# Performance work log

Measured on AMD Instinct MI355X. Metric: run time of the kernel, lower is better.

## Reference

```python
import jax, jax.numpy as jnp
import numpy as np

B, T, H, S = 2, 2048, 16, 64
EMB = H * S  # 1024


def layer_norm(x, g, b, eps=1e-5):
    mu = jnp.mean(x, axis=-1, keepdims=True)
    var = jnp.var(x, axis=-1, keepdims=True)
    return (x - mu) * jax.lax.rsqrt(var + eps) * g + b


def setup_inputs() -> dict:
    key = jax.random.key(0)
    ks = jax.random.split(key, 12)
    sc = 0.02
    return {
        "x": jax.random.normal(ks[0], (B, T, EMB), dtype=jnp.float32),
        "Wkqv": jax.random.normal(ks[1], (S, 3 * S), dtype=jnp.float32) * sc,
        "Wproj": jax.random.normal(ks[2], (EMB, EMB), dtype=jnp.float32) * sc,
        "g1": jnp.ones((EMB,), jnp.float32),
        "b1": jnp.zeros((EMB,), jnp.float32),
        "W1": jax.random.normal(ks[3], (EMB, 4 * EMB), dtype=jnp.float32) * sc,
        "bff1": jnp.zeros((4 * EMB,), jnp.float32),
        "W2": jax.random.normal(ks[4], (4 * EMB, EMB), dtype=jnp.float32) * sc,
        "bff2": jnp.zeros((EMB,), jnp.float32),
        "g2": jnp.ones((EMB,), jnp.float32),
        "b2": jnp.zeros((EMB,), jnp.float32),
    }


def reference(x, Wkqv, Wproj, g1, b1, W1, bff1, W2, bff2, g2, b2):
    Bb, Tt, _ = x.shape
    xh = x.reshape(Bb, Tt, H, S)                     # [B,T,H,S]
    kqv = jnp.einsum('bths,sd->bthd', xh, Wkqv)      # [B,T,H,3S], shared per-head weight
    k, q, v = jnp.split(kqv, 3, axis=-1)             # note order: k, q, v
    scores = jnp.einsum('bihk,bjhk->bijh', q, k) / jnp.sqrt(jnp.float32(S))
    att = jax.nn.softmax(scores, axis=2)             # softmax over key dim j
    res = jnp.einsum('btih,bihs->bths', att, v).reshape(Bb, Tt, EMB)
    mha = res @ Wproj                                # Linear(emb, emb, bias=False)
    x = layer_norm(x + mha, g1, b1)
    h = jax.nn.gelu(x @ W1 + bff1, approximate=False)
    ff = h @ W2 + bff2
    return layer_norm(x + ff, g2, b2)
```

## Files before the change

kernel.cpp:

```cpp
#include <hip/hip_runtime.h>
#include <hip/hip_bf16.h>
#include <math.h>

#define B_ 2
#define T_ 2048
#define H_ 16
#define S_ 64
#define EMB 1024
#define FF 4096
#define BT (B_*T_)
#define ROWS (B_*T_*H_)

typedef __attribute__((ext_vector_type(8))) short s16x8;
typedef __attribute__((ext_vector_type(4))) float f32x4;

struct P4 { unsigned short* p[4]; };

__device__ __forceinline__ unsigned short f2b(float f) {
    return __builtin_bit_cast(unsigned short, __float2bfloat16(f));
}
__device__ __forceinline__ float b2f(short u) {
    return __builtin_bit_cast(float, ((unsigned int)(unsigned short)u) << 16);
}

__device__ __forceinline__ void gl_lds16(const void* g, void* l) {
    __builtin_amdgcn_global_load_lds(
        (const __attribute__((address_space(1))) void*)g,
        (__attribute__((address_space(3))) void*)l, 16, 0, 0);
}

__device__ __forceinline__ f32x4 mfma16(s16x8 a, s16x8 b, f32x4 c) {
    return __builtin_amdgcn_mfma_f32_16x16x32_bf16(a, b, c, 0, 0, 0);
}

#define WAIT_VM8 0x0F78
#define WAIT_VM0 0x0F70

__global__ __launch_bounds__(256) void kqv_kernel(const float* __restrict__ x,
        const unsigned short* __restrict__ Wqt, unsigned short* __restrict__ K,
        unsigned short* __restrict__ Q, unsigned short* __restrict__ V) {
    const int tid = threadIdx.x;
    const int w = tid >> 6, lane = tid & 63;
    const int l15 = lane & 15, quad = lane >> 4;
    const long r0 = (long)blockIdx.x * 128 + w * 32;

    s16x8 af[2][2];
    #pragma unroll
    for (int mt = 0; mt < 2; ++mt)
        #pragma unroll
        for (int ks = 0; ks < 2; ++ks) {
            const float* xp = x + (r0 + mt*16 + l15) * 64 + ks*32 + quad*8;
            const float4 v0 = *(const float4*)xp;
            const float4 v1 = *(const float4*)(xp + 4);
            s16x8 a;
            a[0] = (short)f2b(v0.x); a[1] = (short)f2b(v0.y);
            a[2] = (short)f2b(v0.z); a[3] = (short)f2b(v0.w);
            a[4] = (short)f2b(v1.x); a[5] = (short)f2b(v1.y);
            a[6] = (short)f2b(v1.z); a[7] = (short)f2b(v1.w);
            af[mt][ks] = a;
        }

    #pragma unroll
    for (int nt = 0; nt < 12; ++nt) {
        const s16x8 b0 = *(const s16x8*)&Wqt[(nt*16 + l15)*64 + quad*8];
        const s16x8 b1 = *(const s16x8*)&Wqt[(nt*16 + l15)*64 + 32 + quad*8];
        f32x4 acc[2] = {};
        #pragma unroll
        for (int mt = 0; mt < 2; ++mt) {
            acc[mt] = mfma16(af[mt][0], b0, acc[mt]);
            acc[mt] = mfma16(af[mt][1], b1, acc[mt]);
        }
        unsigned short* dst = (nt < 4) ? K : (nt < 8) ? Q : V;
        const int c0 = (nt & 3) * 16 + l15;
        #pragma unroll
        for (int mt = 0; mt < 2; ++mt)
            #pragma unroll
            for (int r = 0; r < 4; ++r)
                dst[(r0 + mt*16 + quad*4 + r) * 64 + c0] = f2b(acc[mt][r]);
    }
}

__global__ __launch_bounds__(256) void vt_kernel(const unsigned short* __restrict__ V,
        unsigned short* __restrict__ VT) {
    __shared__ unsigned short Ts[64][72];
    const int tid = threadIdx.x;
    const int tt = blockIdx.x, bh = blockIdx.y;
    const int b = bh >> 4, h = bh & 15;
    const long vbase = ((long)b * (T_*H_) + h) * 64;
    #pragma unroll
    for (int i = 0; i < 2; ++i) {
        const int id = i * 256 + tid;
        const int tr = id >> 3, dc = (id & 7) * 8;
        const s16x8 v = *(const s16x8*)&V[vbase + (long)(tt*64 + tr)*1024 + dc];
        *(s16x8*)&Ts[tr][dc] = v;
    }
    __syncthreads();
    #pragma unroll
    for (int i = 0; i < 2; ++i) {
        const int id = i * 256 + tid;
        const int d = id >> 3, tc = (id & 7) * 8;
        s16x8 o;
        #pragma unroll
        for (int j = 0; j < 8; ++j) o[j] = (short)Ts[tc + j][d];
        *(s16x8*)&VT[((long)bh*64 + d)*2048 + tt*64 + tc] = o;
    }
}

__global__ __launch_bounds__(64, 2) void attn_kernel(const unsigned short* __restrict__ Q,
        const unsigned short* __restrict__ K, const unsigned short* __restrict__ VT,
        unsigned short* __restrict__ res) {
    __shared__ __align__(16) unsigned short Kbuf[2][2][32*32];
    __shared__ __align__(16) unsigned short Vbuf[2][64*32];
    __shared__ __align__(16) unsigned short Ps[32*36];
    const int lane = threadIdx.x;
    const int l15 = lane & 15, quad = lane >> 4;
    const int bid = blockIdx.x;
    const int qt = bid & 63, bh = bid >> 6;
    const int b = bh >> 4, h = bh & 15;
    const long base = ((long)b * (T_*H_) + h) * 64;
    const unsigned short* Qp = Q + base;
    const unsigned short* Kp = K + base;
    const unsigned short* Vp = VT + (long)bh * 64 * 2048;
    const int q0 = qt * 32;

    s16x8 qf[2][2];
    #pragma unroll
    for (int qq = 0; qq < 2; ++qq)
        #pragma unroll
        for (int ks = 0; ks < 2; ++ks) {
            const s16x8 raw = *(const s16x8*)&Qp[(long)(q0 + qq*16 + l15)*1024 + ks*32 + quad*8];
            s16x8 q;
            #pragma unroll
            for (int j = 0; j < 8; ++j) q[j] = (short)f2b(b2f(raw[j]) * 0.125f);
            qf[qq][ks] = q;
        }

    s16x8 onef;
    #pragma unroll
    for (int j = 0; j < 8; ++j) onef[j] = (short)0x3F80;

    f32x4 oacc[2][4] = {};
    f32x4 lacc[2] = {};

    const int j16 = lane >> 2;
    const int c8  = (lane & 3) * 8;

    auto stage = [&](int bufi, int kt) {
        const unsigned short* kg = Kp + (long)(kt*32) * 1024;
        char* kl = (char*)&Kbuf[bufi][0][0];
        gl_lds16(kg + (long)j16*1024 + c8,           kl +    0 + lane*16);
        gl_lds16(kg + (long)(j16+16)*1024 + c8,      kl + 1024 + lane*16);
        gl_lds16(kg + (long)j16*1024 + 32 + c8,      kl + 2048 + lane*16);
        gl_lds16(kg + (long)(j16+16)*1024 + 32 + c8, kl + 3072 + lane*16);
        const unsigned short* vg = Vp + kt*32 + c8;
        char* vl = (char*)&Vbuf[bufi][0];
        gl_lds16(vg + (long)(j16     )*2048, vl +    0 + lane*16);
        gl_lds16(vg + (long)(j16 + 16)*2048, vl + 1024 + lane*16);
        gl_lds16(vg + (long)(j16 + 32)*2048, vl + 2048 + lane*16);
        gl_lds16(vg + (long)(j16 + 48)*2048, vl + 3072 + lane*16);
    };

    auto compute = [&](int bufi) {
        f32x4 sT[2][2] = {};
        #pragma unroll
        for (int ks = 0; ks < 2; ++ks)
            #pragma unroll
            for (int jt = 0; jt < 2; ++jt) {
                const s16x8 kf = *(const s16x8*)&Kbuf[bufi][ks][(jt*16 + l15)*32 + quad*8];
                sT[jt][0] = mfma16(kf, qf[0][ks], sT[jt][0]);
                sT[jt][1] = mfma16(kf, qf[1][ks], sT[jt][1]);
            }
        #pragma unroll
        for (int jt = 0; jt < 2; ++jt)
            #pragma unroll
            for (int qq = 0; qq < 2; ++qq) {
                uint2 pk;
                pk.x = (unsigned int)f2b(__expf(sT[jt][qq][0]))
                     | ((unsigned int)f2b(__expf(sT[jt][qq][1])) << 16);
                pk.y = (unsigned int)f2b(__expf(sT[jt][qq][2]))
                     | ((unsigned int)f2b(__expf(sT[jt][qq][3])) << 16);
                *(uint2*)&Ps[(qq*16 + l15)*36 + jt*16 + quad*4] = pk;
            }
        s16x8 pf[2];
        #pragma unroll
        for (int qq = 0; qq < 2; ++qq) {
            pf[qq] = *(const s16x8*)&Ps[(qq*16 + l15)*36 + quad*8];
            lacc[qq] = mfma16(pf[qq], onef, lacc[qq]);
        }
        #pragma unroll
        for (int nt = 0; nt < 4; ++nt) {
            const s16x8 vf = *(const s16x8*)&Vbuf[bufi][(nt*16 + l15)*32 + quad*8];
            oacc[0][nt] = mfma16(pf[0], vf, oacc[0][nt]);
            oacc[1][nt] = mfma16(pf[1], vf, oacc[1][nt]);
        }
    };

    stage(0, 0);
    for (int kt = 0; kt < 63; ++kt) {
        stage((kt + 1) & 1, kt + 1);
        __builtin_amdgcn_s_waitcnt(WAIT_VM8);
        __builtin_amdgcn_sched_barrier(0);
        compute(kt & 1);
    }
    __builtin_amdgcn_s_waitcnt(WAIT_VM0);
    __builtin_amdgcn_sched_barrier(0);
    compute(1);

    #pragma unroll
    for (int qq = 0; qq < 2; ++qq)
        #pragma unroll
        for (int r = 0; r < 4; ++r) {
            const float inv = 1.f / lacc[qq][r];
            const int t = q0 + qq*16 + quad*4 + r;
            #pragma unroll
            for (int nt = 0; nt < 4; ++nt)
                res[((long)(b*T_ + t))*EMB + h*64 + nt*16 + l15] =
                    f2b(oacc[qq][nt][r] * inv);
        }
}

__global__ __launch_bounds__(256) void gemm_gelu(const unsigned short* __restrict__ A,
        const unsigned short* __restrict__ Bt, const float* __restrict__ bias,
        unsigned short* __restrict__ C, int M, int N, int Kd) {
    __shared__ __align__(16) unsigned short As[128 * 32];
    __shared__ __align__(16) unsigned short Bs[128 * 32];
    const int tid = threadIdx.x;
    const int w = tid >> 6, lane = tid & 63;
    const int l15 = lane & 15, quad = lane >> 4;
    const int wm = w >> 1, wn = w & 1;
    const int bn = blockIdx.x, bm = blockIdx.y;
    const int sr = lane >> 2, skq = lane & 3;
    f32x4 acc[4][4] = {};
    const long arow = (long)(bm*128 + w*32 + sr);
    const long brow = (long)(bn*128 + w*32 + sr);

    for (int kt = 0; kt < Kd; kt += 32) {
        gl_lds16(A  + (arow     )*Kd + kt + skq*8, (char*)As + (w*32     )*64 + lane*16);
        gl_lds16(A  + (arow + 16)*Kd + kt + skq*8, (char*)As + (w*32 + 16)*64 + lane*16);
        gl_lds16(Bt + (brow     )*Kd + kt + skq*8, (char*)Bs + (w*32     )*64 + lane*16);
        gl_lds16(Bt + (brow + 16)*Kd + kt + skq*8, (char*)Bs + (w*32 + 16)*64 + lane*16);
        __syncthreads();
        s16x8 af[4], bf[4];
        #pragma unroll
        for (int mt = 0; mt < 4; ++mt)
            af[mt] = *(const s16x8*)&As[(wm*64 + mt*16 + l15)*32 + quad*8];
        #pragma unroll
        for (int nt = 0; nt < 4; ++nt)
            bf[nt] = *(const s16x8*)&Bs[(wn*64 + nt*16 + l15)*32 + quad*8];
        #pragma unroll
        for (int mt = 0; mt < 4; ++mt)
            #pragma unroll
            for (int nt = 0; nt < 4; ++nt)
                acc[mt][nt] = mfma16(af[mt], bf[nt], acc[mt][nt]);
        __syncthreads();
    }

    #pragma unroll
    for (int mt = 0; mt < 4; ++mt) {
        const int row0 = bm*128 + wm*64 + mt*16 + quad*4;
        #pragma unroll
        for (int nt = 0; nt < 4; ++nt) {
            const int col = bn*128 + wn*64 + nt*16 + l15;
            const float bv = bias[col];
            #pragma unroll
            for (int r = 0; r < 4; ++r) {
                float v = acc[mt][nt][r] + bv;
                v = 0.5f * v * (1.f + erff(v * 0.70710678118654752440f));
                C[(long)(row0 + r)*N + col] = f2b(v);
            }
        }
    }
}

__global__ __launch_bounds__(256) void gemm_splitk(const unsigned short* __restrict__ A,
        const unsigned short* __restrict__ Bt, P4 parts, int M, int N, int Kd, int Ks) {
    __shared__ __align__(16) unsigned short As[128 * 32];
    __shared__ __align__(16) unsigned short Bs[128 * 32];
    const int tid = threadIdx.x;
    const int w = tid >> 6, lane = tid & 63;
    const int l15 = lane & 15, quad = lane >> 4;
    const int wm = w >> 1, wn = w & 1;
    const int bn = blockIdx.x, bm = blockIdx.y, s = blockIdx.z;
    const int sr = lane >> 2, skq = lane & 3;
    f32x4 acc[4][4] = {};
    const long arow = (long)(bm*128 + w*32 + sr);
    const long brow = (long)(bn*128 + w*32 + sr);
    const int k0 = s * Ks;

    for (int kt = k0; kt < k0 + Ks; kt += 32) {
        gl_lds16(A  + (arow     )*Kd + kt + skq*8, (char*)As + (w*32     )*64 + lane*16);
        gl_lds16(A  + (arow + 16)*Kd + kt + skq*8, (char*)As + (w*32 + 16)*64 + lane*16);
        gl_lds16(Bt + (brow     )*Kd + kt + skq*8, (char*)Bs + (w*32     )*64 + lane*16);
        gl_lds16(Bt + (brow + 16)*Kd + kt + skq*8, (char*)Bs + (w*32 + 16)*64 + lane*16);
        __syncthreads();
        s16x8 af[4], bf[4];
        #pragma unroll
        for (int mt = 0; mt < 4; ++mt)
            af[mt] = *(const s16x8*)&As[(wm*64 + mt*16 + l15)*32 + quad*8];
        #pragma unroll
        for (int nt = 0; nt < 4; ++nt)
            bf[nt] = *(const s16x8*)&Bs[(wn*64 + nt*16 + l15)*32 + quad*8];
        #pragma unroll
        for (int mt = 0; mt < 4; ++mt)
            #pragma unroll
            for (int nt = 0; nt < 4; ++nt)
                acc[mt][nt] = mfma16(af[mt], bf[nt], acc[mt][nt]);
        __syncthreads();
    }

    unsigned short* Cp = parts.p[s];
    #pragma unroll
    for (int mt = 0; mt < 4; ++mt) {
        const int row0 = bm*128 + wm*64 + mt*16 + quad*4;
        #pragma unroll
        for (int nt = 0; nt < 4; ++nt) {
            const int col = bn*128 + wn*64 + nt*16 + l15;
            #pragma unroll
            for (int r = 0; r < 4; ++r)
                Cp[(long)(row0 + r)*N + col] = f2b(acc[mt][nt][r]);
        }
    }
}

template <int P, int XBF>
__global__ __launch_bounds__(256) void ln_kernel(const void* __restrict__ xa,
        P4 parts, const float* __restrict__ addb, const float* __restrict__ g,
        const float* __restrict__ bia, float* __restrict__ out,
        unsigned short* __restrict__ outb) {
    const int row = blockIdx.x;
    const int tid = threadIdx.x;
    float4 v;
    if (XBF) {
        const ushort4 u = ((const ushort4*)xa)[(long)row * (EMB/4) + tid];
        v.x = b2f((short)u.x); v.y = b2f((short)u.y);
        v.z = b2f((short)u.z); v.w = b2f((short)u.w);
    } else {
        v = ((const float4*)xa)[(long)row * (EMB/4) + tid];
    }
    #pragma unroll
    for (int p = 0; p < P; ++p) {
        const ushort4 u = ((const ushort4*)(parts.p[p] + (long)row * EMB))[tid];
        v.x += b2f((short)u.x); v.y += b2f((short)u.y);
        v.z += b2f((short)u.z); v.w += b2f((short)u.w);
    }
    if (addb) {
        const float4 ab = ((const float4*)addb)[tid];
        v.x += ab.x; v.y += ab.y; v.z += ab.z; v.w += ab.w;
    }
    float s = v.x + v.y + v.z + v.w;
    float ss = v.x * v.x + v.y * v.y + v.z * v.z + v.w * v.w;
    #pragma unroll
    for (int off = 32; off > 0; off >>= 1) {
        s += __shfl_down(s, off, 64);
        ss += __shfl_down(ss, off, 64);
    }
    __shared__ float ls[4], lss[4];
    __shared__ float mean_s, rstd_s;
    const int wid = tid >> 6, lane = tid & 63;
    if (lane == 0) { ls[wid] = s; lss[wid] = ss; }
    __syncthreads();
    if (tid == 0) {
        const float S0 = ls[0] + ls[1] + ls[2] + ls[3];
        const float S2 = lss[0] + lss[1] + lss[2] + lss[3];
        const float mean = S0 * (1.f / EMB);
        const float var = S2 * (1.f / EMB) - mean * mean;
        mean_s = mean;
        rstd_s = rsqrtf(var + 1e-5f);
    }
    __syncthreads();
    const float mean = mean_s, rstd = rstd_s;
    const float4 gg = ((const float4*)g)[tid];
    const float4 bb = ((const float4*)bia)[tid];
    float4 o;
    o.x = (v.x - mean) * rstd * gg.x + bb.x;
    o.y = (v.y - mean) * rstd * gg.y + bb.y;
    o.z = (v.z - mean) * rstd * gg.z + bb.z;
    o.w = (v.w - mean) * rstd * gg.w + bb.w;
    if (out) ((float4*)(out + (long)row * EMB))[tid] = o;
    if (outb) {
        unsigned short* ob = outb + (long)row * EMB + tid * 4;
        ob[0] = f2b(o.x); ob[1] = f2b(o.y); ob[2] = f2b(o.z); ob[3] = f2b(o.w);
    }
}

__global__ __launch_bounds__(256) void transp_all(const float* __restrict__ Wp,
        const float* __restrict__ W1, const float* __restrict__ W2,
        const float* __restrict__ Wq, unsigned short* __restrict__ Wpt,
        unsigned short* __restrict__ W1t, unsigned short* __restrict__ W2t,
        unsigned short* __restrict__ Wqt) {
    int id = blockIdx.x;
    const float* W; unsigned short* Wt; int Kd, N, ntx;
    if (id < 1024)      {            W = Wp; Wt = Wpt; Kd = 1024; N = 1024; ntx = 32; }
    else if (id < 5120) { id -= 1024; W = W1; Wt = W1t; Kd = 1024; N = 4096; ntx = 128; }
    else if (id < 9216) { id -= 5120; W = W2; Wt = W2t; Kd = 4096; N = 1024; ntx = 32; }
    else                { id -= 9216; W = Wq; Wt = Wqt; Kd = 64;   N = 192;  ntx = 6;  }
    __shared__ float Ts[32][33];
    const int tid = threadIdx.x;
    const int n0 = (id % ntx) * 32, k0 = (id / ntx) * 32;
    const int r = tid >> 3, c4 = (tid & 7) * 4;
    const float4 v = *(const float4*)&W[(long)(k0 + r) * N + n0 + c4];
    Ts[r][c4] = v.x; Ts[r][c4 + 1] = v.y; Ts[r][c4 + 2] = v.z; Ts[r][c4 + 3] = v.w;
    __syncthreads();
    #pragma unroll
    for (int i = 0; i < 4; ++i)
        Wt[(long)(n0 + r) * Kd + k0 + c4 + i] = f2b(Ts[c4 + i][r]);
}

extern "C" void kernel_launch(void* const* d_in, const int* in_sizes, int n_in,
                              void* d_out, int out_size, void* d_ws, size_t ws_size,
                              hipStream_t stream) {
    (void)in_sizes; (void)n_in; (void)out_size;
    const float* x     = (const float*)d_in[0];
    const float* Wkqv  = (const float*)d_in[1];
    const float* Wproj = (const float*)d_in[2];
    const float* g1    = (const float*)d_in[3];
    const float* b1    = (const float*)d_in[4];
    const float* W1    = (const float*)d_in[5];
    const float* bff1  = (const float*)d_in[6];
    const float* W2    = (const float*)d_in[7];
    const float* bff2  = (const float*)d_in[8];
    const float* g2    = (const float*)d_in[9];
    const float* b2    = (const float*)d_in[10];
    float* out = (float*)d_out;
    char* ws = (char*)d_ws;

    const size_t MB = 1u << 20;
    unsigned short* Qb   = (unsigned short*)(ws + 0 * MB);
    unsigned short* Kb   = (unsigned short*)(ws + 8 * MB);
    unsigned short* Vb   = (unsigned short*)(ws + 16 * MB);
    unsigned short* resb = (unsigned short*)(ws + 24 * MB);
    unsigned short* hb   = (unsigned short*)(ws + 8 * MB);
    unsigned short* VTb  = (unsigned short*)(ws + 40 * MB);
    unsigned short* mp0  = (unsigned short*)(ws + 40 * MB);
    unsigned short* mp1  = (unsigned short*)(ws + 48 * MB);
    unsigned short* x1b  = Qb;
    unsigned short* Wpt  = (unsigned short*)(ws + 72 * MB);
    unsigned short* W1t  = (unsigned short*)(ws + 74 * MB);
    unsigned short* W2t  = (unsigned short*)(ws + 82 * MB);
    unsigned short* Wqt  = (unsigned short*)(ws + 90 * MB);
    unsigned short* fp2  = (unsigned short*)(ws + 91 * MB);
    unsigned short* fp3  = (unsigned short*)(ws + 99 * MB);
    const bool big = ws_size >= 108 * MB;

    transp_all<<<dim3(9228), 256, 0, stream>>>(Wproj, W1, W2, Wkqv, Wpt, W1t, W2t, Wqt);

    kqv_kernel<<<dim3(ROWS/128), 256, 0, stream>>>(x, Wqt, Kb, Qb, Vb);
    vt_kernel<<<dim3(T_/64, B_*H_), 256, 0, stream>>>(Vb, VTb);
    attn_kernel<<<dim3(2048), 64, 0, stream>>>(Qb, Kb, VTb, resb);
    P4 mp; mp.p[0] = mp0; mp.p[1] = mp1; mp.p[2] = nullptr; mp.p[3] = nullptr;
    gemm_splitk<<<dim3(EMB/128, BT/128, 2), 256, 0, stream>>>(resb, Wpt, mp, BT, EMB, EMB, EMB/2);
    ln_kernel<2, 0><<<dim3(BT), 256, 0, stream>>>(x, mp, nullptr, g1, b1, nullptr, x1b);
    gemm_gelu<<<dim3(FF/128, BT/128), 256, 0, stream>>>(x1b, W1t, bff1, hb, BT, FF, EMB);
    if (big) {
        P4 fp; fp.p[0] = mp0; fp.p[1] = mp1; fp.p[2] = fp2; fp.p[3] = fp3;
        gemm_splitk<<<dim3(EMB/128, BT/128, 4), 256, 0, stream>>>(hb, W2t, fp, BT, EMB, FF, FF/4);
        ln_kernel<4, 1><<<dim3(BT), 256, 0, stream>>>(x1b, fp, bff2, g2, b2, out, nullptr);
    } else {
        P4 fp; fp.p[0] = mp0; fp.p[1] = mp1; fp.p[2] = nullptr; fp.p[3] = nullptr;
        gemm_splitk<<<dim3(EMB/128, BT/128, 2), 256, 0, stream>>>(hb, W2t, fp, BT, EMB, FF, FF/2);
        ln_kernel<2, 1><<<dim3(BT), 256, 0, stream>>>(x1b, fp, bff2, g2, b2, out, nullptr);
    }
}
```

Before: 361.3 us.

## Load attention K/V tiles directly into registers with double-buffered prefetch

Replaces the LDS staging of K and V tiles (global_load_lds plus explicit waitcnt and sched barriers) with direct global-to-register loads. Two register sets are ping-ponged so the next tile's loads are issued while the current tile is computed. The occupancy hint in launch_bounds is dropped, and the bf16 pack switches from rounding to truncation of the exp values. This cuts LDS traffic and the manual wait bookkeeping, but uses more VGPRs, leaves latency hiding to the compiler, and truncation slightly changes numerics.

```diff
diff --git a/kernel.cpp b/kernel.cpp
--- a/kernel.cpp
+++ b/kernel.cpp
@@ -22,6 +22,11 @@
 __device__ __forceinline__ float b2f(short u) {
     return __builtin_bit_cast(float, ((unsigned int)(unsigned short)u) << 16);
 }
+__device__ __forceinline__ unsigned int pk2t(float a, float b) {
+    const unsigned ua = __builtin_bit_cast(unsigned, a);
+    const unsigned ub = __builtin_bit_cast(unsigned, b);
+    return (ub & 0xffff0000u) | (ua >> 16);
+}
 
 __device__ __forceinline__ void gl_lds16(const void* g, void* l) {
     __builtin_amdgcn_global_load_lds(
@@ -32,9 +37,6 @@
 __device__ __forceinline__ f32x4 mfma16(s16x8 a, s16x8 b, f32x4 c) {
     return __builtin_amdgcn_mfma_f32_16x16x32_bf16(a, b, c, 0, 0, 0);
 }
-
-#define WAIT_VM8 0x0F78
-#define WAIT_VM0 0x0F70
 
 __global__ __launch_bounds__(256) void kqv_kernel(const float* __restrict__ x,
         const unsigned short* __restrict__ Wqt, unsigned short* __restrict__ K,
@@ -106,12 +108,10 @@
     }
 }
 
-__global__ __launch_bounds__(64, 2) void attn_kernel(const unsigned short* __restrict__ Q,
+__global__ __launch_bounds__(64) void attn_kernel(const unsigned short* __restrict__ Q,
         const unsigned short* __restrict__ K, const unsigned short* __restrict__ VT,
         unsigned short* __restrict__ res) {
-    __shared__ __align__(16) unsigned short Kbuf[2][2][32*32];
-    __shared__ __align__(16) unsigned short Vbuf[2][64*32];
-    __shared__ __align__(16) unsigned short Ps[32*36];
+    __shared__ __align__(16) unsigned short Ps[32 * 36];
     const int lane = threadIdx.x;
     const int l15 = lane & 15, quad = lane >> 4;
     const int bid = blockIdx.x;
@@ -142,43 +142,41 @@
     f32x4 oacc[2][4] = {};
     f32x4 lacc[2] = {};
 
-    const int j16 = lane >> 2;
-    const int c8  = (lane & 3) * 8;
-
-    auto stage = [&](int bufi, int kt) {
-        const unsigned short* kg = Kp + (long)(kt*32) * 1024;
-        char* kl = (char*)&Kbuf[bufi][0][0];
-        gl_lds16(kg + (long)j16*1024 + c8,           kl +    0 + lane*16);
-        gl_lds16(kg + (long)(j16+16)*1024 + c8,      kl + 1024 + lane*16);
-        gl_lds16(kg + (long)j16*1024 + 32 + c8,      kl + 2048 + lane*16);
-        gl_lds16(kg + (long)(j16+16)*1024 + 32 + c8, kl + 3072 + lane*16);
-        const unsigned short* vg = Vp + kt*32 + c8;
-        char* vl = (char*)&Vbuf[bufi][0];
-        gl_lds16(vg + (long)(j16     )*2048, vl +    0 + lane*16);
-        gl_lds16(vg + (long)(j16 + 16)*2048, vl + 1024 + lane*16);
-        gl_lds16(vg + (long)(j16 + 32)*2048, vl + 2048 + lane*16);
-        gl_lds16(vg + (long)(j16 + 48)*2048, vl + 3072 + lane*16);
+    const unsigned short* kA = Kp + (long)l15 * 1024 + quad * 8;
+    const unsigned short* vA = Vp + (long)l15 * 2048 + quad * 8;
+
+    s16x8 k0[4], v0[4], k1[4], v1[4];
+
+    auto loadK = [&](s16x8* kf, int kt) {
+        const unsigned short* p = kA + (long)kt * 32768;
+        kf[0] = *(const s16x8*)(p);
+        kf[1] = *(const s16x8*)(p + 32);
+        kf[2] = *(const s16x8*)(p + 16*1024);
+        kf[3] = *(const s16x8*)(p + 16*1024 + 32);
     };
-
-    auto compute = [&](int bufi) {
+    auto loadV = [&](s16x8* vf, int kt) {
+        const unsigned short* p = vA + kt * 32;
+        vf[0] = *(const s16x8*)(p);
+        vf[1] = *(const s16x8*)(p + 16*2048);
+        vf[2] = *(const s16x8*)(p + 32*2048);
+        vf[3] = *(const s16x8*)(p + 48*2048);
+    };
+    auto compute = [&](const s16x8* kf, const s16x8* vf) {
         f32x4 sT[2][2] = {};
         #pragma unroll
         for (int ks = 0; ks < 2; ++ks)
             #pragma unroll
             for (int jt = 0; jt < 2; ++jt) {
-                const s16x8 kf = *(const s16x8*)&Kbuf[bufi][ks][(jt*16 + l15)*32 + quad*8];
-                sT[jt][0] = mfma16(kf, qf[0][ks], sT[jt][0]);
-                sT[jt][1] = mfma16(kf, qf[1][ks], sT[jt][1]);
+                sT[jt][0] = mfma16(kf[jt*2 + ks], qf[0][ks], sT[jt][0]);
+                sT[jt][1] = mfma16(kf[jt*2 + ks], qf[1][ks], sT[jt][1]);
             }
         #pragma unroll
         for (int jt = 0; jt < 2; ++jt)
             #pragma unroll
             for (int qq = 0; qq < 2; ++qq) {
                 uint2 pk;
-                pk.x = (unsigned int)f2b(__expf(sT[jt][qq][0]))
-                     | ((unsigned int)f2b(__expf(sT[jt][qq][1])) << 16);
-                pk.y = (unsigned int)f2b(__expf(sT[jt][qq][2]))
-                     | ((unsigned int)f2b(__expf(sT[jt][qq][3])) << 16);
+                pk.x = pk2t(__expf(sT[jt][qq][0]), __expf(sT[jt][qq][1]));
+                pk.y = pk2t(__expf(sT[jt][qq][2]), __expf(sT[jt][qq][3]));
                 *(uint2*)&Ps[(qq*16 + l15)*36 + jt*16 + quad*4] = pk;
             }
         s16x8 pf[2];
@@ -189,22 +187,19 @@
         }
         #pragma unroll
         for (int nt = 0; nt < 4; ++nt) {
-            const s16x8 vf = *(const s16x8*)&Vbuf[bufi][(nt*16 + l15)*32 + quad*8];
-            oacc[0][nt] = mfma16(pf[0], vf, oacc[0][nt]);
-            oacc[1][nt] = mfma16(pf[1], vf, oacc[1][nt]);
+            oacc[0][nt] = mfma16(pf[0], vf[nt], oacc[0][nt]);
+            oacc[1][nt] = mfma16(pf[1], vf[nt], oacc[1][nt]);
         }
     };
 
-    stage(0, 0);
-    for (int kt = 0; kt < 63; ++kt) {
-        stage((kt + 1) & 1, kt + 1);
-        __builtin_amdgcn_s_waitcnt(WAIT_VM8);
-        __builtin_amdgcn_sched_barrier(0);
-        compute(kt & 1);
-    }
-    __builtin_amdgcn_s_waitcnt(WAIT_VM0);
-    __builtin_amdgcn_sched_barrier(0);
-    compute(1);
+    loadK(k0, 0); loadV(v0, 0);
+    loadK(k1, 1); loadV(v1, 1);
+    for (int kt = 0; kt < 64; kt += 2) {
+        compute(k0, v0);
+        if (kt + 2 < 64) { loadK(k0, kt + 2); loadV(v0, kt + 2); }
+        compute(k1, v1);
+        if (kt + 3 < 64) { loadK(k1, kt + 3); loadV(v1, kt + 3); }
+    }
 
     #pragma unroll
     for (int qq = 0; qq < 2; ++qq)
```

Result: slower. 411.2 us (+13.8%).
